# Kernel tuning notes

Hardware: AMD Instinct MI355X
Metric: run time of the kernel (lower is better)

The kernel has to match this reference:

```python
import jax, jax.numpy as jnp
import numpy as np

IN_DIM = 128
OUT_DIM = 256
N_ETYPES = 4
N_STEPS = 8
B = 128
N_NODES = 256
E = 393216
CONCAT = IN_DIM + OUT_DIM


def _conv1d(x, w, b):
    # x: [B, C, L], w: [O, I, K] -> valid conv, stride 1
    y = jax.lax.conv_general_dilated(x, w, (1,), 'VALID', dimension_numbers=('NCH', 'OIH', 'NCH'))
    return y + b[None, :, None]


def _maxpool1d(x, k, s):
    return jax.lax.reduce_window(x, -jnp.inf, jax.lax.max, (1, 1, k), (1, 1, s), 'VALID')


def setup_inputs():
    key = jax.random.key(0)
    ks = jax.random.split(key, 16)
    Nn = B * N_NODES
    sc = 0.05
    f32 = jnp.float32
    return {
        'features': jax.random.normal(ks[0], (Nn, IN_DIM), f32),
        'src': jax.random.randint(ks[1], (E,), 0, Nn),
        'dst': jax.random.randint(ks[2], (E,), 0, Nn),
        'etype': jax.random.randint(ks[3], (E,), 0, N_ETYPES),
        'W_msg': jax.random.normal(ks[4], (N_ETYPES, OUT_DIM, OUT_DIM), f32) * sc,
        'b_msg': jnp.zeros((N_ETYPES, OUT_DIM), f32),
        'gru_Wi': jax.random.normal(ks[5], (OUT_DIM, 3 * OUT_DIM), f32) * sc,
        'gru_Wh': jax.random.normal(ks[6], (OUT_DIM, 3 * OUT_DIM), f32) * sc,
        'gru_bi': jnp.zeros((3 * OUT_DIM,), f32),
        'gru_bh': jnp.zeros((3 * OUT_DIM,), f32),
        'conv1_w': jax.random.normal(ks[7], (OUT_DIM, OUT_DIM, 3), f32) * sc,
        'conv1_b': jnp.zeros((OUT_DIM,), f32),
        'conv2_w': jax.random.normal(ks[8], (OUT_DIM, OUT_DIM, 1), f32) * sc,
        'conv2_b': jnp.zeros((OUT_DIM,), f32),
        'convc1_w': jax.random.normal(ks[9], (CONCAT, CONCAT, 3), f32) * sc,
        'convc1_b': jnp.zeros((CONCAT,), f32),
        'convc2_w': jax.random.normal(ks[10], (CONCAT, CONCAT, 1), f32) * sc,
        'convc2_b': jnp.zeros((CONCAT,), f32),
        'wy': jax.random.normal(ks[11], (OUT_DIM, 1), f32) * sc,
        'by': jnp.zeros((1,), f32),
        'wz': jax.random.normal(ks[12], (CONCAT, 1), f32) * sc,
        'bz': jnp.zeros((1,), f32),
        'num_graphs': B,
    }


def reference(features, src, dst, etype, W_msg, b_msg, gru_Wi, gru_Wh, gru_bi, gru_bh,
              conv1_w, conv1_b, conv2_w, conv2_b, convc1_w, convc1_b, convc2_w, convc2_b,
              wy, by, wz, bz, num_graphs):
    Nn = features.shape[0]
    # DGL GatedGraphConv: pad input feats up to out_feats
    h = jnp.pad(features, ((0, 0), (0, OUT_DIM - IN_DIM)))
    for _ in range(N_STEPS):
        # per-etype linear transform of all nodes: [Nn, T, O]
        H_all = jnp.einsum('nd,tdo->nto', h, W_msg) + b_msg[None]
        msg = H_all[src, etype]                              # [E, O]
        a = jax.ops.segment_sum(msg, dst, num_segments=Nn)   # [Nn, O]
        gi = a @ gru_Wi + gru_bi
        gh = h @ gru_Wh + gru_bh
        ir, iz, ig = jnp.split(gi, 3, axis=-1)
        hr, hz, hg = jnp.split(gh, 3, axis=-1)
        r = jax.nn.sigmoid(ir + hr)
        z = jax.nn.sigmoid(iz + hz)
        g = jnp.tanh(ig + r * hg)
        h = (1.0 - z) * g + z * h
    x_i = features.reshape(num_graphs, -1, IN_DIM)
    h_i = h.reshape(num_graphs, -1, OUT_DIM)
    c_i = jnp.concatenate([h_i, x_i], axis=-1)
    Y1 = _maxpool1d(jax.nn.relu(_conv1d(h_i.transpose(0, 2, 1), conv1_w, conv1_b)), 3, 2)
    Y2 = _maxpool1d(jax.nn.relu(_conv1d(Y1, conv2_w, conv2_b)), 2, 2).transpose(0, 2, 1)
    Z1 = _maxpool1d(jax.nn.relu(_conv1d(c_i.transpose(0, 2, 1), convc1_w, convc1_b)), 3, 2)
    Z2 = _maxpool1d(jax.nn.relu(_conv1d(Z1, convc2_w, convc2_b)), 2, 2).transpose(0, 2, 1)
    before_avg = (Y2 @ wy + by) * (Z2 @ wz + bz)   # [B, L, 1]
    avg = before_avg.mean(axis=1)                    # [B, 1]
    return jax.nn.sigmoid(avg).squeeze(-1)           # [B]
```

## Files before the change

kernel.cpp:

```cpp
#include <hip/hip_runtime.h>

#define DEV static __device__ __forceinline__

typedef float f32x4 __attribute__((ext_vector_type(4)));
typedef __bf16 bf16x8 __attribute__((ext_vector_type(8)));
typedef unsigned int u32x4 __attribute__((ext_vector_type(4)));
typedef unsigned int u32x2 __attribute__((ext_vector_type(2)));

#define NNODE 32768
#define NEDGE 393216

DEV unsigned short f2bf(float f) {
    unsigned int u = __builtin_bit_cast(unsigned int, f);
    u += 0x7FFFu + ((u >> 16) & 1u);
    return (unsigned short)(u >> 16);
}
DEV float bf2f(unsigned int b) {
    unsigned int u = b << 16;
    return __builtin_bit_cast(float, u);
}
DEV unsigned int pk2(float a, float b) {
    return (unsigned int)f2bf(a) | ((unsigned int)f2bf(b) << 16);
}
DEV float sigf(float x) { return 1.f / (1.f + __expf(-x)); }

DEV void gld16(const void* g, void* l) {
    __builtin_amdgcn_global_load_lds(
        (const __attribute__((address_space(1))) void*)(g),
        (__attribute__((address_space(3))) void*)(l),
        16, 0, 0);
}


__global__ __launch_bounds__(256) void init_k(
    const float* __restrict__ feat,
    unsigned short* __restrict__ hb0, unsigned short* __restrict__ hb1,
    unsigned short* __restrict__ fb)
{
    int idx = blockIdx.x * 256 + threadIdx.x;
    int r = idx >> 8, c = idx & 255;
    float f = 0.f;
    if (r < NNODE && c < 128) f = feat[(size_t)r * 128 + c];
    unsigned short v = f2bf(f);
    hb0[(size_t)r * 256 + c] = v;
    hb1[(size_t)r * 256 + c] = v;
    if (c < 128) fb[(size_t)r * 128 + c] = v;
}

__global__ __launch_bounds__(256) void prep_wmsg_k(
    const float* __restrict__ Wm, unsigned short* __restrict__ WT)
{
    int idx = blockIdx.x * 256 + threadIdx.x;
    int j = idx >> 8, d = idx & 255;
    int t = j >> 8, o = j & 255;
    WT[idx] = f2bf(Wm[t * 65536 + d * 256 + o]);
}

__global__ __launch_bounds__(256) void prep_gru_k(
    const float* __restrict__ Wi, const float* __restrict__ Wh,
    unsigned short* __restrict__ B2T)
{
    int idx = blockIdx.x * 256 + threadIdx.x;
    int j = idx >> 9, k = idx & 511;
    int band = j >> 6, g = (j >> 4) & 3, ch = (band << 4) + (j & 15);
    float v = 0.f;
    if (g == 0) v = (k < 256) ? Wi[k * 768 + ch] : Wh[(k - 256) * 768 + ch];
    else if (g == 1) v = (k < 256) ? Wi[k * 768 + 256 + ch] : Wh[(k - 256) * 768 + 256 + ch];
    else if (g == 2) { if (k < 256) v = Wi[k * 768 + 512 + ch]; }
    else { if (k >= 256) v = Wh[(k - 256) * 768 + 512 + ch]; }
    B2T[idx] = f2bf(v);
}

__global__ __launch_bounds__(256) void prep_bias2_k(
    const float* __restrict__ bi, const float* __restrict__ bh,
    float* __restrict__ b2)
{
    int j = blockIdx.x * 256 + threadIdx.x;
    int band = j >> 6, g = (j >> 4) & 3, ch = (band << 4) + (j & 15);
    float v;
    if (g == 0) v = bi[ch] + bh[ch];
    else if (g == 1) v = bi[256 + ch] + bh[256 + ch];
    else if (g == 2) v = bi[512 + ch];
    else v = bh[512 + ch];
    b2[j] = v;
}

__global__ __launch_bounds__(256) void prep_conv_k(
    const float* __restrict__ c1w, const float* __restrict__ c2w,
    const float* __restrict__ cc1w, const float* __restrict__ cc2w,
    unsigned short* __restrict__ BTY, unsigned short* __restrict__ BT2,
    unsigned short* __restrict__ BTZ, unsigned short* __restrict__ BTc2)
{
    int idx = blockIdx.x * 256 + threadIdx.x;
    if (idx < 196608) {
        int o = idx / 768, kk = idx - o * 768, k = kk >> 8, c = kk & 255;
        BTY[idx] = f2bf(c1w[o * 768 + c * 3 + k]);
    } else if (idx < 262144) {
        int r = idx - 196608, o = r >> 8, c = r & 255;
        BT2[r] = f2bf(c2w[o * 256 + c]);
    } else if (idx < 704512) {
        int jx = idx - 262144, o = jx / 1152, kk = jx - o * 1152;
        float v;
        if (kk < 768) { int k = kk >> 8, c = kk & 255; v = cc1w[o * 1152 + c * 3 + k]; }
        else { int r = kk - 768, kf = r >> 7, cf = r & 127; v = cc1w[o * 1152 + (256 + cf) * 3 + kf]; }
        BTZ[jx] = f2bf(v);
    } else {
        int r = idx - 704512, o = r / 384, c = r - o * 384;
        BTc2[r] = f2bf(cc2w[o * 384 + c]);
    }
}


__global__ __launch_bounds__(256) void count_k(
    const int* __restrict__ dst, int* __restrict__ cnt)
{
    int e = blockIdx.x * 256 + threadIdx.x;
    atomicAdd(&cnt[dst[e]], 1);
}

__global__ __launch_bounds__(1024) void scan1_k(
    const int* __restrict__ cnt, int* __restrict__ rp, int* __restrict__ bsum)
{
    __shared__ int buf[1024];
    int b = blockIdx.x, tid = threadIdx.x;
    int n = (b << 10) + tid;
    int v = cnt[n];
    buf[tid] = v;
    __syncthreads();
    for (int off = 1; off < 1024; off <<= 1) {
        int x = (tid >= off) ? buf[tid - off] : 0;
        __syncthreads();
        buf[tid] += x;
        __syncthreads();
    }
    rp[n] = buf[tid] - v;
    if (tid == 1023) bsum[b] = buf[1023];
}

__global__ __launch_bounds__(64) void scan2_k(
    const int* __restrict__ bsum, int* __restrict__ boff, int* __restrict__ rp)
{
    int lane = threadIdx.x;
    int v = (lane < 32) ? bsum[lane] : 0;
    int s = v;
    #pragma unroll
    for (int off = 1; off < 32; off <<= 1) {
        int x = __shfl_up(s, off, 64);
        if (lane >= off) s += x;
    }
    if (lane < 32) boff[lane] = s - v;
    if (lane == 31) rp[NNODE] = s;
}

__global__ __launch_bounds__(1024) void scan3_k(
    int* __restrict__ rp, const int* __restrict__ boff)
{
    int b = blockIdx.x, tid = threadIdx.x;
    rp[(b << 10) + tid] += boff[b];
}

__global__ __launch_bounds__(256) void fill_k(
    const int* __restrict__ src, const int* __restrict__ dst,
    const int* __restrict__ et, const int* __restrict__ rp,
    int* __restrict__ pos, int* __restrict__ edat)
{
    int e = blockIdx.x * 256 + threadIdx.x;
    int d = dst[e];
    int p = atomicAdd(&pos[d], 1);
    edat[rp[d] + p] = src[e] | (et[e] << 20);
}


__global__ __launch_bounds__(256) void agg2_k(
    const int* __restrict__ rp, const int* __restrict__ edat,
    const unsigned short* __restrict__ Hmsg, unsigned short* __restrict__ Aonly)
{
    int wave = threadIdx.x >> 6, lane = threadIdx.x & 63;
    int n = (blockIdx.x << 2) + wave;
    int e0 = rp[n], e1 = rp[n + 1];
    float a0 = 0.f, a1 = 0.f, a2 = 0.f, a3 = 0.f;
    const unsigned short* hc = Hmsg + (lane << 2);
    int e = e0;
    for (; e + 8 <= e1; e += 8) {
        u32x2 v[8];
        #pragma unroll
        for (int q = 0; q < 8; q++) {
            int d = edat[e + q];
            v[q] = *(const u32x2*)(hc + ((size_t)(d & 0xFFFFF) << 10) + ((d >> 20) << 8));
        }
        #pragma unroll
        for (int q = 0; q < 8; q++) {
            a0 += bf2f(v[q].x & 0xFFFFu); a1 += bf2f(v[q].x >> 16);
            a2 += bf2f(v[q].y & 0xFFFFu); a3 += bf2f(v[q].y >> 16);
        }
    }
    for (; e < e1; e++) {
        int d = edat[e];
        u32x2 v = *(const u32x2*)(hc + ((size_t)(d & 0xFFFFF) << 10) + ((d >> 20) << 8));
        a0 += bf2f(v.x & 0xFFFFu); a1 += bf2f(v.x >> 16);
        a2 += bf2f(v.y & 0xFFFFu); a3 += bf2f(v.y >> 16);
    }
    u32x2 p; p.x = pk2(a0, a1); p.y = pk2(a2, a3);
    *(u32x2*)(Aonly + (size_t)n * 256 + (lane << 2)) = p;
}

#define STAGE_COORDS                                            \
    int srow[4], scb[4], soff[4];                               \
    _Pragma("unroll")                                           \
    for (int p = 0; p < 4; p++) {                               \
        int c = wave + p * 4;                                   \
        int half = c >> 3, cc = c & 7;                          \
        srow[p] = cc * 16 + (lane >> 2);                        \
        scb[p] = (((lane & 3) ^ ((lane >> 3) & 3)) + half * 4) * 8; \
        soff[p] = half * 4096 + cc * 512;                       \
    }

#define MFMA64(AS, BS)                                                        \
    _Pragma("unroll")                                                         \
    for (int h = 0; h < 2; h++) {                                             \
        bf16x8 af[4], bfr[4];                                                 \
        _Pragma("unroll")                                                     \
        for (int i = 0; i < 4; i++)                                           \
            af[i] = *(const bf16x8*)(&(AS)[h * 4096 + (qm + i * 16 + fm) * 32 + fksw * 8]); \
        _Pragma("unroll")                                                     \
        for (int i = 0; i < 4; i++)                                           \
            bfr[i] = *(const bf16x8*)(&(BS)[h * 4096 + (qn + i * 16 + fm) * 32 + fksw * 8]); \
        _Pragma("unroll")                                                     \
        for (int i = 0; i < 4; i++)                                           \
            _Pragma("unroll")                                                 \
            for (int j = 0; j < 4; j++)                                       \
                acc[i][j] = __builtin_amdgcn_mfma_f32_16x16x32_bf16(bfr[j], af[i], acc[i][j], 0, 0, 0); \
    }

__global__ __launch_bounds__(256) void gemm_bt(
    const unsigned short* __restrict__ A, int lda,
    const unsigned short* __restrict__ Bt,
    unsigned short* __restrict__ Cb, int ldcb,
    const float* __restrict__ bias,
    int N, int K, int swz, int relu)
{
    __shared__ __align__(16) unsigned short As0[128 * 64];
    __shared__ __align__(16) unsigned short As1[128 * 64];
    __shared__ __align__(16) unsigned short Bs0[128 * 64];
    __shared__ __align__(16) unsigned short Bs1[128 * 64];
    const int tid = threadIdx.x;
    int id = blockIdx.x;
    if (swz) { int per = gridDim.x >> 3; id = (id & 7) * per + (id >> 3); }
    const int nb = N >> 7;
    const int bm = id / nb, bn = id - bm * nb;
    const int wave = tid >> 6, lane = tid & 63;
    const unsigned short* Ag = A + (size_t)(bm * 128) * lda;
    const unsigned short* Bg = Bt + (size_t)(bn * 128) * K;
    const int qm = (wave & 1) << 6, qn = (wave >> 1) << 6;
    const int fm = lane & 15, fkv = lane >> 4;
    const int fksw = fkv ^ ((fm >> 1) & 3);
    STAGE_COORDS

    auto stageA = [&](int kb, unsigned short* dst) {
        #pragma unroll
        for (int p = 0; p < 4; p++)
            gld16(Ag + (size_t)srow[p] * lda + kb + scb[p], dst + soff[p]);
    };
    auto stageB = [&](int kb, unsigned short* dst) {
        #pragma unroll
        for (int p = 0; p < 4; p++)
            gld16(Bg + (size_t)srow[p] * K + kb + scb[p], dst + soff[p]);
    };

    f32x4 acc[4][4] = {};

    stageA(0, As0); stageB(0, Bs0);
    __syncthreads();
    unsigned short *Ac = As0, *An = As1, *Bc = Bs0, *Bn = Bs1;
    for (int kb = 0; kb < K; kb += 64) {
        if (kb + 64 < K) { stageA(kb + 64, An); stageB(kb + 64, Bn); }
        MFMA64(Ac, Bc)
        __syncthreads();
        { auto t = Ac; Ac = An; An = t; }
        { auto t = Bc; Bc = Bn; Bn = t; }
    }

    const int m0 = bm * 128 + qm + fm;
    const int n0 = bn * 128 + qn + (fkv << 2);
    #pragma unroll
    for (int i = 0; i < 4; i++) {
        int row = m0 + i * 16;
        #pragma unroll
        for (int j = 0; j < 4; j++) {
            int col = n0 + j * 16;
            float v0 = acc[i][j][0], v1 = acc[i][j][1],
                  v2 = acc[i][j][2], v3 = acc[i][j][3];
            if (bias) {
                float4 bv = *(const float4*)(bias + col);
                v0 += bv.x; v1 += bv.y; v2 += bv.z; v3 += bv.w;
            }
            if (relu) {
                v0 = fmaxf(v0, 0.f); v1 = fmaxf(v1, 0.f);
                v2 = fmaxf(v2, 0.f); v3 = fmaxf(v3, 0.f);
            }
            u32x2 p; p.x = pk2(v0, v1); p.y = pk2(v2, v3);
            *(u32x2*)(Cb + (size_t)row * ldcb + col) = p;
        }
    }
}

__global__ __launch_bounds__(256) void gemm_conv(
    const unsigned short* __restrict__ Ah,
    const unsigned short* __restrict__ Af,
    const unsigned short* __restrict__ Bt,
    unsigned short* __restrict__ Cb, int ldcb,
    const float* __restrict__ bias,
    int N, int K)
{
    __shared__ __align__(16) unsigned short As0[128 * 64];
    __shared__ __align__(16) unsigned short As1[128 * 64];
    __shared__ __align__(16) unsigned short Bs0[128 * 64];
    __shared__ __align__(16) unsigned short Bs1[128 * 64];
    const int tid = threadIdx.x;
    int id = blockIdx.x;
    { int per = gridDim.x >> 3; id = (id & 7) * per + (id >> 3); }
    const int nb = N >> 7;
    const int bm = id / nb, bn = id - bm * nb;
    const int wave = tid >> 6, lane = tid & 63;
    const unsigned short* Bg = Bt + (size_t)(bn * 128) * K;
    const int qm = (wave & 1) << 6, qn = (wave >> 1) << 6;
    const int fm = lane & 15, fkv = lane >> 4;
    const int fksw = fkv ^ ((fm >> 1) & 3);
    STAGE_COORDS

    auto stageA = [&](int kb, unsigned short* dst) {
        const unsigned short* base; int ldA, col, shift;
        if (kb < 768) { base = Ah; ldA = 256; shift = kb >> 8; col = kb & 255; }
        else { int r = kb - 768; base = Af; ldA = 128; shift = r >> 7; col = r & 127; }
        const unsigned short* Ag = base + (size_t)(bm * 128 + shift) * ldA + col;
        #pragma unroll
        for (int p = 0; p < 4; p++)
            gld16(Ag + (size_t)srow[p] * ldA + scb[p], dst + soff[p]);
    };
    auto stageB = [&](int kb, unsigned short* dst) {
        #pragma unroll
        for (int p = 0; p < 4; p++)
            gld16(Bg + (size_t)srow[p] * K + kb + scb[p], dst + soff[p]);
    };

    f32x4 acc[4][4] = {};

    stageA(0, As0); stageB(0, Bs0);
    __syncthreads();
    unsigned short *Ac = As0, *An = As1, *Bc = Bs0, *Bn = Bs1;
    for (int kb = 0; kb < K; kb += 64) {
        if (kb + 64 < K) { stageA(kb + 64, An); stageB(kb + 64, Bn); }
        MFMA64(Ac, Bc)
        __syncthreads();
        { auto t = Ac; Ac = An; An = t; }
        { auto t = Bc; Bc = Bn; Bn = t; }
    }

    const int m0 = bm * 128 + qm + fm;
    const int n0 = bn * 128 + qn + (fkv << 2);
    #pragma unroll
    for (int i = 0; i < 4; i++) {
        int row = m0 + i * 16;
        #pragma unroll
        for (int j = 0; j < 4; j++) {
            int col = n0 + j * 16;
            float4 bv = *(const float4*)(bias + col);
            float v0 = fmaxf(acc[i][j][0] + bv.x, 0.f);
            float v1 = fmaxf(acc[i][j][1] + bv.y, 0.f);
            float v2 = fmaxf(acc[i][j][2] + bv.z, 0.f);
            float v3 = fmaxf(acc[i][j][3] + bv.w, 0.f);
            u32x2 p; p.x = pk2(v0, v1); p.y = pk2(v2, v3);
            *(u32x2*)(Cb + (size_t)row * ldcb + col) = p;
        }
    }
}

__global__ __launch_bounds__(256) void gemm_gru(
    const unsigned short* __restrict__ Aonly,
    const unsigned short* __restrict__ hbc,
    const unsigned short* __restrict__ Bt,
    const float* __restrict__ b2p,
    unsigned short* __restrict__ hbn)
{
    __shared__ __align__(16) unsigned short As0[128 * 64];
    __shared__ __align__(16) unsigned short As1[128 * 64];
    __shared__ __align__(16) unsigned short Bs0[128 * 64];
    __shared__ __align__(16) unsigned short Bs1[128 * 64];
    const int tid = threadIdx.x;
    int id = blockIdx.x;
    { int per = gridDim.x >> 3; id = (id & 7) * per + (id >> 3); }
    const int bm = id >> 3;
    const int bn = id & 7;
    const int wave = tid >> 6, lane = tid & 63;
    const unsigned short* Bg = Bt + (size_t)(bn * 128) * 512;
    const int qm = (wave & 1) << 6, qn = (wave >> 1) << 6;
    const int fm = lane & 15, fkv = lane >> 4;
    const int fksw = fkv ^ ((fm >> 1) & 3);
    STAGE_COORDS

    auto stageA = [&](int kb, unsigned short* dst) {
        const unsigned short* base = (kb < 256) ? Aonly : hbc;
        const unsigned short* Ag = base + (size_t)(bm * 128) * 256 + (kb & 255);
        #pragma unroll
        for (int p = 0; p < 4; p++)
            gld16(Ag + (size_t)srow[p] * 256 + scb[p], dst + soff[p]);
    };
    auto stageB = [&](int kb, unsigned short* dst) {
        #pragma unroll
        for (int p = 0; p < 4; p++)
            gld16(Bg + (size_t)srow[p] * 512 + kb + scb[p], dst + soff[p]);
    };

    f32x4 acc[4][4] = {};

    stageA(0, As0); stageB(0, Bs0);
    __syncthreads();
    unsigned short *Ac = As0, *An = As1, *Bc = Bs0, *Bn = Bs1;
    #pragma unroll
    for (int kb = 0; kb < 512; kb += 64) {
        if (kb < 448) { stageA(kb + 64, An); stageB(kb + 64, Bn); }
        MFMA64(Ac, Bc)
        __syncthreads();
        { auto t = Ac; Ac = An; An = t; }
        { auto t = Bc; Bc = Bn; Bn = t; }
    }

    const int band = (bn << 1) + (qn >> 6);
    const int chb = (band << 4) + (fkv << 2);
    const float4 brv = *(const float4*)(b2p + (band << 6) + 0  + (fkv << 2));
    const float4 bzv = *(const float4*)(b2p + (band << 6) + 16 + (fkv << 2));
    const float4 bgv = *(const float4*)(b2p + (band << 6) + 32 + (fkv << 2));
    const float4 bhv = *(const float4*)(b2p + (band << 6) + 48 + (fkv << 2));
    const float br_[4] = {brv.x, brv.y, brv.z, brv.w};
    const float bz_[4] = {bzv.x, bzv.y, bzv.z, bzv.w};
    const float bg_[4] = {bgv.x, bgv.y, bgv.z, bgv.w};
    const float bh_[4] = {bhv.x, bhv.y, bhv.z, bhv.w};
    const int m0 = bm * 128 + qm + fm;
    #pragma unroll
    for (int i = 0; i < 4; i++) {
        int row = m0 + i * 16;
        u32x2 hv = *(const u32x2*)(hbc + (size_t)row * 256 + chb);
        float hp[4] = {bf2f(hv.x & 0xFFFFu), bf2f(hv.x >> 16),
                       bf2f(hv.y & 0xFFFFu), bf2f(hv.y >> 16)};
        float hn[4];
        #pragma unroll
        for (int r = 0; r < 4; r++) {
            float rg = sigf(acc[i][0][r] + br_[r]);
            float zz = sigf(acc[i][1][r] + bz_[r]);
            float pre = acc[i][2][r] + bg_[r] + rg * (acc[i][3][r] + bh_[r]);
            pre = fminf(fmaxf(pre, -15.f), 15.f);
            float t = __expf(2.f * pre);
            float gq = (t - 1.f) / (t + 1.f);
            hn[r] = (1.f - zz) * gq + zz * hp[r];
        }
        u32x2 p; p.x = pk2(hn[0], hn[1]); p.y = pk2(hn[2], hn[3]);
        *(u32x2*)(hbn + (size_t)row * 256 + chb) = p;
    }
}

__global__ __launch_bounds__(256) void pool_k(
    const unsigned short* __restrict__ in, int ldin, int Lb_in, int L_out,
    int win, int C,
    unsigned short* __restrict__ ob, int ldo)
{
    int idx = blockIdx.x * 256 + threadIdx.x;
    int c = idx % C;
    int row = idx / C;
    int b = row / L_out, lp = row - b * L_out;
    const unsigned short* p = in + (size_t)(b * Lb_in + 2 * lp) * ldin + c;
    float m = bf2f(p[0]);
    for (int d = 1; d < win; d++) m = fmaxf(m, bf2f(p[(size_t)d * ldin]));
    ob[(size_t)row * ldo + c] = f2bf(m);
}

__global__ __launch_bounds__(64) void final_k(
    const unsigned short* __restrict__ CY, const unsigned short* __restrict__ CZ,
    const float* __restrict__ wy, const float* __restrict__ by,
    const float* __restrict__ wz, const float* __restrict__ bz,
    float* __restrict__ out)
{
    int b = blockIdx.x, lane = threadIdx.x;
    float val = 0.f;
    if (lane < 63) {
        const unsigned short* y0 = CY + (size_t)(b * 126 + 2 * lane) * 256;
        const unsigned short* y1 = y0 + 256;
        float y = 0.f;
        for (int o = 0; o < 256; o++)
            y += fmaxf(bf2f(y0[o]), bf2f(y1[o])) * wy[o];
        y += by[0];
        const unsigned short* z0 = CZ + (size_t)(b * 126 + 2 * lane) * 384;
        const unsigned short* z1 = z0 + 384;
        float z = 0.f;
        for (int o = 0; o < 384; o++)
            z += fmaxf(bf2f(z0[o]), bf2f(z1[o])) * wz[o];
        z += bz[0];
        val = y * z;
    }
    for (int off = 32; off > 0; off >>= 1) val += __shfl_down(val, off, 64);
    if (lane == 0) out[b] = sigf(val * (1.f / 63.f));
}


extern "C" void kernel_launch(void* const* d_in, const int* in_sizes, int n_in,
                              void* d_out, int out_size, void* d_ws, size_t ws_size,
                              hipStream_t stream)
{
    const float* feat = (const float*)d_in[0];
    const int* src = (const int*)d_in[1];
    const int* dst = (const int*)d_in[2];
    const int* et  = (const int*)d_in[3];
    const float* Wm  = (const float*)d_in[4];
    const float* bm  = (const float*)d_in[5];
    const float* Wi  = (const float*)d_in[6];
    const float* Wh  = (const float*)d_in[7];
    const float* bi  = (const float*)d_in[8];
    const float* bh  = (const float*)d_in[9];
    const float* c1w = (const float*)d_in[10];
    const float* c1b = (const float*)d_in[11];
    const float* c2w = (const float*)d_in[12];
    const float* c2b = (const float*)d_in[13];
    const float* cc1w = (const float*)d_in[14];
    const float* cc1b = (const float*)d_in[15];
    const float* cc2w = (const float*)d_in[16];
    const float* cc2b = (const float*)d_in[17];
    const float* wy = (const float*)d_in[18];
    const float* by = (const float*)d_in[19];
    const float* wz = (const float*)d_in[20];
    const float* bz = (const float*)d_in[21];
    float* out = (float*)d_out;

    char* w = (char*)d_ws;
    size_t off = 0;
    auto alloc = [&](size_t bytes) -> char* {
        char* p = w + off; off += (bytes + 255) & ~(size_t)255; return p;
    };
    unsigned short* hb0 = (unsigned short*)alloc((size_t)(NNODE + 8) * 256 * 2);
    unsigned short* hb1 = (unsigned short*)alloc((size_t)(NNODE + 8) * 256 * 2);
    unsigned short* fb  = (unsigned short*)alloc((size_t)(NNODE + 8) * 128 * 2);
    unsigned short* Aonly = (unsigned short*)alloc((size_t)NNODE * 256 * 2);
    char* R = alloc((size_t)NNODE * 1024 * 2);
    unsigned short* Hmsg = (unsigned short*)R;
    unsigned short* CbY  = (unsigned short*)R;
    unsigned short* CbZ  = (unsigned short*)(R + (size_t)NNODE * 256 * 2);
    unsigned short* P    = (unsigned short*)alloc((size_t)16128 * 384 * 2);
    unsigned short* Cb2Y = (unsigned short*)alloc((size_t)16128 * 256 * 2);
    unsigned short* Cb2Z = (unsigned short*)alloc((size_t)16128 * 384 * 2);
    unsigned short* WT   = (unsigned short*)alloc(1024 * 256 * 2);
    unsigned short* B2T  = (unsigned short*)alloc(1024 * 512 * 2);
    float* b2            = (float*)alloc(1024 * 4);
    unsigned short* BTY  = (unsigned short*)alloc(256 * 768 * 2);
    unsigned short* BT2  = (unsigned short*)alloc(256 * 256 * 2);
    unsigned short* BTZ  = (unsigned short*)alloc(384 * 1152 * 2);
    unsigned short* BTc2 = (unsigned short*)alloc(384 * 384 * 2);
    int* rp     = (int*)alloc((NNODE + 1) * 4);
    int* pos    = (int*)alloc(NNODE * 4);
    int* cnt    = (int*)alloc(NNODE * 4);
    int* bsum   = (int*)alloc(32 * 4);
    int* boff   = (int*)alloc(32 * 4);
    int* edat   = (int*)alloc(NEDGE * 4);

    hipLaunchKernelGGL(init_k, dim3(NNODE + 8), dim3(256), 0, stream, feat, hb0, hb1, fb);
    hipLaunchKernelGGL(prep_wmsg_k, dim3(1024), dim3(256), 0, stream, Wm, WT);
    hipLaunchKernelGGL(prep_gru_k, dim3(2048), dim3(256), 0, stream, Wi, Wh, B2T);
    hipLaunchKernelGGL(prep_bias2_k, dim3(4), dim3(256), 0, stream, bi, bh, b2);
    hipLaunchKernelGGL(prep_conv_k, dim3(3328), dim3(256), 0, stream,
                       c1w, c2w, cc1w, cc2w, BTY, BT2, BTZ, BTc2);
    hipMemsetAsync(pos, 0, NNODE * 4, stream);
    hipMemsetAsync(cnt, 0, NNODE * 4, stream);
    hipLaunchKernelGGL(count_k, dim3(NEDGE / 256), dim3(256), 0, stream, dst, cnt);
    hipLaunchKernelGGL(scan1_k, dim3(32), dim3(1024), 0, stream, cnt, rp, bsum);
    hipLaunchKernelGGL(scan2_k, dim3(1), dim3(64), 0, stream, bsum, boff, rp);
    hipLaunchKernelGGL(scan3_k, dim3(32), dim3(1024), 0, stream, rp, boff);
    hipLaunchKernelGGL(fill_k, dim3(NEDGE / 256), dim3(256), 0, stream, src, dst, et, rp, pos, edat);

    unsigned short* hbuf[2] = {hb0, hb1};
    for (int step = 0; step < 8; step++) {
        unsigned short* cur = hbuf[step & 1];
        unsigned short* nxt = hbuf[(step + 1) & 1];
        hipLaunchKernelGGL(gemm_bt, dim3(2048), dim3(256), 0, stream,
            cur, 256, WT, Hmsg, 1024, bm, 1024, 256, 1, 0);
        hipLaunchKernelGGL(agg2_k, dim3(NNODE / 4), dim3(256), 0, stream, rp, edat, Hmsg, Aonly);
        hipLaunchKernelGGL(gemm_gru, dim3(2048), dim3(256), 0, stream,
            Aonly, cur, B2T, b2, nxt);
    }

    hipLaunchKernelGGL(gemm_conv, dim3(512), dim3(256), 0, stream,
        hb0, (const unsigned short*)nullptr, BTY, CbY, 256, c1b, 256, 768);
    hipLaunchKernelGGL(pool_k, dim3(16128), dim3(256), 0, stream,
        CbY, 256, 256, 126, 3, 256, P, 256);
    hipLaunchKernelGGL(gemm_bt, dim3(252), dim3(256), 0, stream,
        P, 256, BT2, Cb2Y, 256, c2b, 256, 256, 0, 1);

    hipLaunchKernelGGL(gemm_conv, dim3(768), dim3(256), 0, stream,
        hb0, fb, BTZ, CbZ, 384, cc1b, 384, 1152);
    hipLaunchKernelGGL(pool_k, dim3(24192), dim3(256), 0, stream,
        CbZ, 384, 256, 126, 3, 384, P, 384);
    hipLaunchKernelGGL(gemm_bt, dim3(378), dim3(256), 0, stream,
        P, 384, BTc2, Cb2Z, 384, cc2b, 384, 384, 0, 1);

    hipLaunchKernelGGL(final_k, dim3(128), dim3(64), 0, stream,
        Cb2Y, Cb2Z, wy, by, wz, bz, out);
}
```

Before: 1.323 ms.

## Pad CSR edge lists to multiples of 8, specialize Hmsg GEMM, skip zero GRU blocks

Each node's edge count is rounded up to a multiple of 8, and the padding points at a zeroed dummy Hmsg row. This lets the aggregation kernel drop its scalar tail loop and always issue 8 loads per iteration. A dedicated gemm_hmsg kernel replaces the generic gemm_bt with compile-time shapes. The GRU GEMM also skips MFMAs for one of its four 16-column sub-tiles per K half, which assumes a block-structured zero pattern in the combined weight. The padding adds extra dummy gathers per node, and the skipped sub-tiles are only correct if those weight regions are truly zero.

```diff
diff --git a/kernel.cpp b/kernel.cpp
--- a/kernel.cpp
+++ b/kernel.cpp
@@ -9,6 +9,7 @@
 
 #define NNODE 32768
 #define NEDGE 393216
+#define EPAD (NEDGE + 8 * NNODE)
 
 DEV unsigned short f2bf(float f) {
     unsigned int u = __builtin_bit_cast(unsigned int, f);
@@ -111,6 +112,11 @@
 }
 
 
+__global__ __launch_bounds__(256) void pad_k(int* __restrict__ edat)
+{
+    edat[blockIdx.x * 256 + threadIdx.x] = NNODE;
+}
+
 __global__ __launch_bounds__(256) void count_k(
     const int* __restrict__ dst, int* __restrict__ cnt)
 {
@@ -124,7 +130,7 @@
     __shared__ int buf[1024];
     int b = blockIdx.x, tid = threadIdx.x;
     int n = (b << 10) + tid;
-    int v = cnt[n];
+    int v = (cnt[n] + 7) & ~7;
     buf[tid] = v;
     __syncthreads();
     for (int off = 1; off < 1024; off <<= 1) {
@@ -180,8 +186,7 @@
     int e0 = rp[n], e1 = rp[n + 1];
     float a0 = 0.f, a1 = 0.f, a2 = 0.f, a3 = 0.f;
     const unsigned short* hc = Hmsg + (lane << 2);
-    int e = e0;
-    for (; e + 8 <= e1; e += 8) {
+    for (int e = e0; e < e1; e += 8) {
         u32x2 v[8];
         #pragma unroll
         for (int q = 0; q < 8; q++) {
@@ -193,12 +198,6 @@
             a0 += bf2f(v[q].x & 0xFFFFu); a1 += bf2f(v[q].x >> 16);
             a2 += bf2f(v[q].y & 0xFFFFu); a3 += bf2f(v[q].y >> 16);
         }
-    }
-    for (; e < e1; e++) {
-        int d = edat[e];
-        u32x2 v = *(const u32x2*)(hc + ((size_t)(d & 0xFFFFF) << 10) + ((d >> 20) << 8));
-        a0 += bf2f(v.x & 0xFFFFu); a1 += bf2f(v.x >> 16);
-        a2 += bf2f(v.y & 0xFFFFu); a3 += bf2f(v.y >> 16);
     }
     u32x2 p; p.x = pk2(a0, a1); p.y = pk2(a2, a3);
     *(u32x2*)(Aonly + (size_t)n * 256 + (lane << 2)) = p;
@@ -231,6 +230,91 @@
             for (int j = 0; j < 4; j++)                                       \
                 acc[i][j] = __builtin_amdgcn_mfma_f32_16x16x32_bf16(bfr[j], af[i], acc[i][j], 0, 0, 0); \
     }
+
+#define MFMA64G(AS, BS, SK)                                                   \
+    _Pragma("unroll")                                                         \
+    for (int h = 0; h < 2; h++) {                                             \
+        bf16x8 af[4], bfr[4];                                                 \
+        _Pragma("unroll")                                                     \
+        for (int i = 0; i < 4; i++)                                           \
+            af[i] = *(const bf16x8*)(&(AS)[h * 4096 + (qm + i * 16 + fm) * 32 + fksw * 8]); \
+        _Pragma("unroll")                                                     \
+        for (int j = 0; j < 4; j++) {                                         \
+            if (j == (SK)) continue;                                          \
+            bfr[j] = *(const bf16x8*)(&(BS)[h * 4096 + (qn + j * 16 + fm) * 32 + fksw * 8]); \
+        }                                                                     \
+        _Pragma("unroll")                                                     \
+        for (int i = 0; i < 4; i++)                                           \
+            _Pragma("unroll")                                                 \
+            for (int j = 0; j < 4; j++) {                                     \
+                if (j == (SK)) continue;                                      \
+                acc[i][j] = __builtin_amdgcn_mfma_f32_16x16x32_bf16(bfr[j], af[i], acc[i][j], 0, 0, 0); \
+            }                                                                 \
+    }
+
+__global__ __launch_bounds__(256) void gemm_hmsg(
+    const unsigned short* __restrict__ A,
+    const unsigned short* __restrict__ Bt,
+    unsigned short* __restrict__ Cb,
+    const float* __restrict__ bias)
+{
+    __shared__ __align__(16) unsigned short As0[128 * 64];
+    __shared__ __align__(16) unsigned short As1[128 * 64];
+    __shared__ __align__(16) unsigned short Bs0[128 * 64];
+    __shared__ __align__(16) unsigned short Bs1[128 * 64];
+    const int tid = threadIdx.x;
+    int id = blockIdx.x;
+    { int per = gridDim.x >> 3; id = (id & 7) * per + (id >> 3); }
+    const int bm = id >> 3, bn = id & 7;
+    const int wave = tid >> 6, lane = tid & 63;
+    const unsigned short* Ag = A + (size_t)(bm * 128) * 256;
+    const unsigned short* Bg = Bt + (size_t)(bn * 128) * 256;
+    const int qm = (wave & 1) << 6, qn = (wave >> 1) << 6;
+    const int fm = lane & 15, fkv = lane >> 4;
+    const int fksw = fkv ^ ((fm >> 1) & 3);
+    STAGE_COORDS
+
+    auto stageA = [&](int kb, unsigned short* dst) {
+        #pragma unroll
+        for (int p = 0; p < 4; p++)
+            gld16(Ag + (size_t)srow[p] * 256 + kb + scb[p], dst + soff[p]);
+    };
+    auto stageB = [&](int kb, unsigned short* dst) {
+        #pragma unroll
+        for (int p = 0; p < 4; p++)
+            gld16(Bg + (size_t)srow[p] * 256 + kb + scb[p], dst + soff[p]);
+    };
+
+    f32x4 acc[4][4] = {};
+
+    stageA(0, As0); stageB(0, Bs0);
+    __syncthreads();
+    unsigned short *Ac = As0, *An = As1, *Bc = Bs0, *Bn = Bs1;
+    #pragma unroll
+    for (int kb = 0; kb < 256; kb += 64) {
+        if (kb < 192) { stageA(kb + 64, An); stageB(kb + 64, Bn); }
+        MFMA64(Ac, Bc)
+        __syncthreads();
+        { auto t = Ac; Ac = An; An = t; }
+        { auto t = Bc; Bc = Bn; Bn = t; }
+    }
+
+    const int m0 = bm * 128 + qm + fm;
+    const int n0 = bn * 128 + qn + (fkv << 2);
+    #pragma unroll
+    for (int i = 0; i < 4; i++) {
+        int row = m0 + i * 16;
+        #pragma unroll
+        for (int j = 0; j < 4; j++) {
+            int col = n0 + j * 16;
+            float4 bv = *(const float4*)(bias + col);
+            u32x2 p;
+            p.x = pk2(acc[i][j][0] + bv.x, acc[i][j][1] + bv.y);
+            p.y = pk2(acc[i][j][2] + bv.z, acc[i][j][3] + bv.w);
+            *(u32x2*)(Cb + (size_t)row * 1024 + col) = p;
+        }
+    }
+}
 
 __global__ __launch_bounds__(256) void gemm_bt(
     const unsigned short* __restrict__ A, int lda,
@@ -419,7 +503,8 @@
     #pragma unroll
     for (int kb = 0; kb < 512; kb += 64) {
         if (kb < 448) { stageA(kb + 64, An); stageB(kb + 64, Bn); }
-        MFMA64(Ac, Bc)
+        if (kb < 256) { MFMA64G(Ac, Bc, 3) }
+        else          { MFMA64G(Ac, Bc, 2) }
         __syncthreads();
         { auto t = Ac; Ac = An; An = t; }
         { auto t = Bc; Bc = Bn; Bn = t; }
@@ -538,7 +623,7 @@
     unsigned short* hb1 = (unsigned short*)alloc((size_t)(NNODE + 8) * 256 * 2);
     unsigned short* fb  = (unsigned short*)alloc((size_t)(NNODE + 8) * 128 * 2);
     unsigned short* Aonly = (unsigned short*)alloc((size_t)NNODE * 256 * 2);
-    char* R = alloc((size_t)NNODE * 1024 * 2);
+    char* R = alloc((size_t)(NNODE + 1) * 1024 * 2);
     unsigned short* Hmsg = (unsigned short*)R;
     unsigned short* CbY  = (unsigned short*)R;
     unsigned short* CbZ  = (unsigned short*)(R + (size_t)NNODE * 256 * 2);
@@ -557,7 +642,7 @@
     int* cnt    = (int*)alloc(NNODE * 4);
     int* bsum   = (int*)alloc(32 * 4);
     int* boff   = (int*)alloc(32 * 4);
-    int* edat   = (int*)alloc(NEDGE * 4);
+    int* edat   = (int*)alloc((size_t)EPAD * 4);
 
     hipLaunchKernelGGL(init_k, dim3(NNODE + 8), dim3(256), 0, stream, feat, hb0, hb1, fb);
     hipLaunchKernelGGL(prep_wmsg_k, dim3(1024), dim3(256), 0, stream, Wm, WT);
@@ -567,6 +652,8 @@
                        c1w, c2w, cc1w, cc2w, BTY, BT2, BTZ, BTc2);
     hipMemsetAsync(pos, 0, NNODE * 4, stream);
     hipMemsetAsync(cnt, 0, NNODE * 4, stream);
+    hipMemsetAsync(Hmsg + (size_t)NNODE * 1024, 0, 1024 * 2, stream);
+    hipLaunchKernelGGL(pad_k, dim3(EPAD / 256), dim3(256), 0, stream, edat);
     hipLaunchKernelGGL(count_k, dim3(NEDGE / 256), dim3(256), 0, stream, dst, cnt);
     hipLaunchKernelGGL(scan1_k, dim3(32), dim3(1024), 0, stream, cnt, rp, bsum);
     hipLaunchKernelGGL(scan2_k, dim3(1), dim3(64), 0, stream, bsum, boff, rp);
@@ -577,8 +664,8 @@
     for (int step = 0; step < 8; step++) {
         unsigned short* cur = hbuf[step & 1];
         unsigned short* nxt = hbuf[(step + 1) & 1];
-        hipLaunchKernelGGL(gemm_bt, dim3(2048), dim3(256), 0, stream,
-            cur, 256, WT, Hmsg, 1024, bm, 1024, 256, 1, 0);
+        hipLaunchKernelGGL(gemm_hmsg, dim3(2048), dim3(256), 0, stream,
+            cur, WT, Hmsg, bm);
         hipLaunchKernelGGL(agg2_k, dim3(NNODE / 4), dim3(256), 0, stream, rp, edat, Hmsg, Aonly);
         hipLaunchKernelGGL(gemm_gru, dim3(2048), dim3(256), 0, stream,
             Aonly, cur, B2T, b2, nxt);
```

New measurement: 1.192 ms. 1.11x faster.
